# Performance work log

Measured on AMD Instinct MI355X. Metric: run time of the kernel, lower is better.

The kernel has to match this reference:

```python
import jax, jax.numpy as jnp
import numpy as np

B, T, C = 2, 2048, 768
H, D = 12, 64
INNER_LR = 0.01


def setup_inputs() -> dict:
    key = jax.random.key(0)
    ks = jax.random.split(key, 5)
    s = 1.0 / np.sqrt(C)
    return {
        "x": jax.random.normal(ks[0], (B, T, C), dtype=jnp.float32),
        "Wq": jax.random.normal(ks[1], (C, C), dtype=jnp.float32) * s,
        "Wk": jax.random.normal(ks[2], (C, C), dtype=jnp.float32) * s,
        "Wv": jax.random.normal(ks[3], (C, C), dtype=jnp.float32) * s,
        "Wo": jax.random.normal(ks[4], (C, C), dtype=jnp.float32) * s,
        "lr_scale": jnp.ones((H, 1, 1), dtype=jnp.float32),
    }


def reference(x, Wq, Wk, Wv, Wo, lr_scale):
    b, t, c = x.shape
    # projections (nn.Linear: x @ W.T), split heads -> [T, B, H, D] for scan
    def proj(W):
        return (x @ W.T).reshape(b, t, H, D).transpose(1, 0, 2, 3)

    q, k, v = proj(Wq), proj(Wk), proj(Wv)
    eff_lr = (INNER_LR * lr_scale)[None]  # [1, H, 1, 1] broadcasts over [B,H,D,D]

    def step(W, qkv_t):
        q_t, k_t, v_t = qkv_t  # each [B, H, D]
        out_t = jnp.einsum('bhij,bhj->bhi', W, q_t)          # read BEFORE update
        err = jnp.einsum('bhij,bhj->bhi', W, k_t) - v_t      # inner-loss residual
        grad = err[..., :, None] * k_t[..., None, :]         # [B,H,D,D] outer product
        W_new = W - eff_lr * grad                            # one GD step on W
        return W_new, out_t

    W0 = jnp.zeros((b, H, D, D), dtype=x.dtype)
    _, outs = jax.lax.scan(step, W0, (q, k, v))              # outs: [T, B, H, D]
    out = outs.transpose(1, 0, 2, 3).reshape(b, t, c)
    return out @ Wo.T
```

## Files before the change

kernel.cpp:

```cpp
#include <hip/hip_runtime.h>

#define BB 2
#define TT 2048
#define CC 768
#define HH 12
#define DD 64
#define NN (BB*TT)
#define NQ (BB*HH*TT*DD)
#define WSZ (CC*CC)
#define NCH 32
#define CL 64
#define NCHUNKS (BB*HH*NCH)

typedef __attribute__((ext_vector_type(8))) short short8;
typedef __attribute__((ext_vector_type(8))) unsigned short ushort8;
typedef __attribute__((ext_vector_type(4))) float f32x4;
typedef unsigned short u16;

#define GLOAD16(g, l)                                                        \
    __builtin_amdgcn_global_load_lds(                                        \
        (const __attribute__((address_space(1))) void*)(g),                  \
        (__attribute__((address_space(3))) void*)(l), 16, 0, 0)

__device__ __forceinline__ u16 f2b(float f) {
    unsigned int u = __builtin_bit_cast(unsigned int, f);
    unsigned int r = (u + 0x7FFFu + ((u >> 16) & 1u)) >> 16;
    return (u16)r;
}
__device__ __forceinline__ float b2f(u16 b) {
    unsigned int u = ((unsigned int)b) << 16;
    return __builtin_bit_cast(float, u);
}
template <int CTRL>
__device__ __forceinline__ float dpp_xadd(float x) {
    int y = __builtin_amdgcn_update_dpp(0, __builtin_bit_cast(int, x),
                                        CTRL, 0xF, 0xF, true);
    return x + __builtin_bit_cast(float, y);
}
__device__ __forceinline__ void st_sw(u16* buf, int row, int col, u16 v) {
    buf[row * 64 + ((((col >> 3) ^ (row & 7)) << 3) | (col & 7))] = v;
}
__device__ __forceinline__ short8 ld_frag(const u16* buf, int row, int lc) {
    return *(const short8*)&buf[row * 64 + ((lc ^ (row & 7)) << 3)];
}
__device__ __forceinline__ short8 gfrag(const u16* base, int row, int lc) {
    return *(const short8*)&base[row * 64 + lc * 8];
}

__global__ __launch_bounds__(256) void cvt5_kernel(
    const float* __restrict__ x,  const float* __restrict__ Wq,
    const float* __restrict__ Wk, const float* __restrict__ Wv,
    const float* __restrict__ Wo,
    u16* __restrict__ xb, u16* __restrict__ wqb, u16* __restrict__ wkb,
    u16* __restrict__ wvb, u16* __restrict__ wob)
{
    const int seg = blockIdx.y;
    const float* s; u16* d; int n8;
    if      (seg == 0) { s = x;  d = xb;  n8 = NQ  / 8; }
    else if (seg == 1) { s = Wq; d = wqb; n8 = WSZ / 8; }
    else if (seg == 2) { s = Wk; d = wkb; n8 = WSZ / 8; }
    else if (seg == 3) { s = Wv; d = wvb; n8 = WSZ / 8; }
    else               { s = Wo; d = wob; n8 = WSZ / 8; }
    int i = blockIdx.x * 256 + threadIdx.x;
    if (i >= n8) return;
    const float* p = s + (size_t)i * 8;
    ushort8 o;
#pragma unroll
    for (int j = 0; j < 8; ++j) o[j] = f2b(p[j]);
    *(ushort8*)(d + (size_t)i * 8) = o;
}

__global__ __launch_bounds__(256) void proj_qkv_kernel(
    const u16* __restrict__ xb,
    const u16* __restrict__ wq, const u16* __restrict__ wk,
    const u16* __restrict__ wv,
    u16* __restrict__ qo, u16* __restrict__ ko, u16* __restrict__ vo)
{
    const int z = blockIdx.z;
    const u16* Bsel = (z == 0) ? wq : ((z == 1) ? wk : wv);
    u16* Osel       = (z == 0) ? qo : ((z == 1) ? ko : vo);

    const int m0 = blockIdx.x * 128;
    const int n0 = blockIdx.y * 128;
    const int tid = threadIdx.x, lane = tid & 63, wid = tid >> 6;
    const int wm = (wid >> 1) * 64, wn = (wid & 1) * 64;

    __shared__ u16 As[128 * 64];
    __shared__ u16 Bs[128 * 64];

    f32x4 acc[4][4];
#pragma unroll
    for (int a = 0; a < 4; ++a)
#pragma unroll
        for (int b = 0; b < 4; ++b) acc[a][b] = (f32x4){0.f, 0.f, 0.f, 0.f};

    for (int kt = 0; kt < CC; kt += 64) {
#pragma unroll
        for (int i = 0; i < 4; ++i) {
            int slot = i * 256 + tid;
            int row = slot >> 3, c = slot & 7;
            int gc = c ^ (row & 7);
            GLOAD16(xb   + (size_t)(m0 + row) * CC + kt + gc * 8,
                    (char*)As + slot * 16);
            GLOAD16(Bsel + (size_t)(n0 + row) * CC + kt + gc * 8,
                    (char*)Bs + slot * 16);
        }
        asm volatile("s_waitcnt vmcnt(0)" ::: "memory");
        __syncthreads();

#pragma unroll
        for (int kh = 0; kh < 2; ++kh) {
            short8 af[4], bf[4];
            const int lc = kh * 4 + (lane >> 4);
#pragma unroll
            for (int mi = 0; mi < 4; ++mi) {
                int row = wm + mi * 16 + (lane & 15);
                af[mi] = *(const short8*)((const char*)As + row * 128
                                          + ((lc ^ (row & 7)) * 16));
            }
#pragma unroll
            for (int ni = 0; ni < 4; ++ni) {
                int row = wn + ni * 16 + (lane & 15);
                bf[ni] = *(const short8*)((const char*)Bs + row * 128
                                          + ((lc ^ (row & 7)) * 16));
            }
#pragma unroll
            for (int mi = 0; mi < 4; ++mi)
#pragma unroll
                for (int ni = 0; ni < 4; ++ni)
                    acc[mi][ni] = __builtin_amdgcn_mfma_f32_16x16x32_bf16(
                        af[mi], bf[ni], acc[mi][ni], 0, 0, 0);
        }
        __syncthreads();
    }

#pragma unroll
    for (int mi = 0; mi < 4; ++mi) {
#pragma unroll
        for (int ni = 0; ni < 4; ++ni) {
            int n = n0 + wn + ni * 16 + (lane & 15);
            int mbase = m0 + wm + mi * 16 + ((lane >> 4) << 2);
            int h = n >> 6, d = n & 63;
#pragma unroll
            for (int r = 0; r < 4; ++r) {
                int m = mbase + r;
                int b = m >> 11, t = m & 2047;
                Osel[(((size_t)b * HH + h) * TT + t) * DD + d] =
                    f2b(acc[mi][ni][r]);
            }
        }
    }
}

__global__ __launch_bounds__(256, 3) void ttt_prep3_kernel(
    const u16* __restrict__ kb, const u16* __restrict__ vb,
    const float* __restrict__ lr_scale,
    u16* __restrict__ ubg, float* __restrict__ pfA, float* __restrict__ pfB,
    u16* __restrict__ mtng, u16* __restrict__ rtng)
{
    const int bx = blockIdx.x;
    const int bh = bx >> 5;
    const int h = bh % HH;
    const float lr = 0.01f * lr_scale[h];
    const u16* kc = kb + (size_t)bx * 4096;
    const u16* vc = vb + (size_t)bx * 4096;
    u16* ubc  = ubg + (size_t)bx * 4096;
    float* pfc = (bx < 384) ? pfA + (size_t)bx * 4096
                            : pfB + (size_t)(bx - 384) * 4096;
    u16* mtnc = mtng + (size_t)bx * 4096;
    u16* rtnc = rtng + (size_t)bx * 4096;

    const int tid = threadIdx.x, lane = tid & 63, wid = tid >> 6;
    const int wm = (wid >> 1) * 32, wn = (wid & 1) * 32;
    const int ar0 = wm + (lane & 15);
    const int br0 = wn + (lane & 15);
    const int lcb = lane >> 4;
    const int or0 = wm + ((lane >> 4) << 2);
    const int oc0 = wn + (lane & 15);

    __shared__ __align__(16) char pool[50176];
    u16* Kl  = (u16*)pool;
    u16* Vl  = (u16*)(pool + 8192);
    u16* KtB = (u16*)(pool + 16384);
    u16* VtB = (u16*)(pool + 24576);
    float (*As)[68] = (float (*)[68])(pool + 32768);
    u16* Rb   = Kl;
    u16* Ub   = Vl;
    u16* TmpB = VtB;
    u16* Tb   = (u16*)(pool + 32768);
    u16* TmpA = (u16*)(pool + 40960);

#pragma unroll
    for (int i = 0; i < 2; ++i) {
        int slot = i * 256 + tid;
        int row = slot >> 3, cc = slot & 7;
        int gc = cc ^ (row & 7);
        GLOAD16(kc + row * 64 + gc * 8, (char*)Kl + slot * 16);
        GLOAD16(vc + row * 64 + gc * 8, (char*)Vl + slot * 16);
    }
    asm volatile("s_waitcnt vmcnt(0)" ::: "memory");
    __syncthreads();

    {
        short8 idA[2][2];
#pragma unroll
        for (int mi = 0; mi < 2; ++mi)
#pragma unroll
            for (int kh = 0; kh < 2; ++kh) {
                short8 idf = {0, 0, 0, 0, 0, 0, 0, 0};
#pragma unroll
                for (int e = 0; e < 8; ++e)
                    if (kh * 32 + lcb * 8 + e == ar0 + mi * 16)
                        idf[e] = (short)0x3F80;
                idA[mi][kh] = idf;
            }

        f32x4 aA[2][2], aKt[2][2], aVt[2][2];
#pragma unroll
        for (int a = 0; a < 2; ++a)
#pragma unroll
            for (int b = 0; b < 2; ++b) {
                aA[a][b]  = (f32x4){0.f, 0.f, 0.f, 0.f};
                aKt[a][b] = (f32x4){0.f, 0.f, 0.f, 0.f};
                aVt[a][b] = (f32x4){0.f, 0.f, 0.f, 0.f};
            }
#pragma unroll
        for (int kh = 0; kh < 2; ++kh) {
            short8 ka[2], kbb[2], vbb[2];
#pragma unroll
            for (int i = 0; i < 2; ++i) {
                ka[i]  = ld_frag(Kl, ar0 + i * 16, kh * 4 + lcb);
                kbb[i] = ld_frag(Kl, br0 + i * 16, kh * 4 + lcb);
                vbb[i] = ld_frag(Vl, br0 + i * 16, kh * 4 + lcb);
            }
#pragma unroll
            for (int mi = 0; mi < 2; ++mi)
#pragma unroll
                for (int ni = 0; ni < 2; ++ni) {
                    aA[mi][ni] = __builtin_amdgcn_mfma_f32_16x16x32_bf16(
                        ka[mi], kbb[ni], aA[mi][ni], 0, 0, 0);
                    aKt[mi][ni] = __builtin_amdgcn_mfma_f32_16x16x32_bf16(
                        idA[mi][kh], kbb[ni], aKt[mi][ni], 0, 0, 0);
                    aVt[mi][ni] = __builtin_amdgcn_mfma_f32_16x16x32_bf16(
                        idA[mi][kh], vbb[ni], aVt[mi][ni], 0, 0, 0);
                }
        }
#pragma unroll
        for (int mi = 0; mi < 2; ++mi)
#pragma unroll
            for (int ni = 0; ni < 2; ++ni)
#pragma unroll
                for (int r = 0; r < 4; ++r) {
                    int t = or0 + mi * 16 + r, s = oc0 + ni * 16;
                    As[t][s] = (t > s) ? lr * aA[mi][ni][r] : 0.f;
                    st_sw(KtB, t, s, f2b(aKt[mi][ni][r]));
                    st_sw(VtB, t, s, f2b(aVt[mi][ni][r]));
                }
    }
    __syncthreads();

    const int j = wid * 16 + (lane >> 2), g = lane & 3;
    float Treg[16];
#pragma unroll
    for (int m = 0; m < 16; ++m) Treg[m] = 0.f;
#pragma unroll
    for (int t = 0; t < 64; ++t) {
        float sum = 0.f;
#pragma unroll
        for (int m = 0; m <= (t >> 2); ++m)
            sum += As[t][g + 4 * m] * Treg[m];
        sum = dpp_xadd<0xB1>(sum);
        sum = dpp_xadd<0x4E>(sum);
        float v = ((t == j) ? 1.f : 0.f) - sum;
        if ((t & 3) == g) Treg[t >> 2] = v;
    }
    __syncthreads();

#pragma unroll
    for (int m = 0; m < 16; ++m) st_sw(Tb, g + 4 * m, j, f2b(Treg[m]));
    __syncthreads();

    {
        f32x4 aR[2][2], aU[2][2], aRt[2][2];
#pragma unroll
        for (int a = 0; a < 2; ++a)
#pragma unroll
            for (int b = 0; b < 2; ++b) {
                aR[a][b]  = (f32x4){0.f, 0.f, 0.f, 0.f};
                aU[a][b]  = (f32x4){0.f, 0.f, 0.f, 0.f};
                aRt[a][b] = (f32x4){0.f, 0.f, 0.f, 0.f};
            }
#pragma unroll
        for (int kh = 0; kh < 2; ++kh) {
            short8 kta[2], vta[2], ta[2], tbf[2], ktb[2];
#pragma unroll
            for (int i = 0; i < 2; ++i) {
                kta[i] = ld_frag(KtB, ar0 + i * 16, kh * 4 + lcb);
                vta[i] = ld_frag(VtB, ar0 + i * 16, kh * 4 + lcb);
                ta[i]  = ld_frag(Tb,  ar0 + i * 16, kh * 4 + lcb);
                tbf[i] = ld_frag(Tb,  br0 + i * 16, kh * 4 + lcb);
                ktb[i] = ld_frag(KtB, br0 + i * 16, kh * 4 + lcb);
            }
#pragma unroll
            for (int mi = 0; mi < 2; ++mi)
#pragma unroll
                for (int ni = 0; ni < 2; ++ni) {
                    aR[mi][ni] = __builtin_amdgcn_mfma_f32_16x16x32_bf16(
                        kta[mi], tbf[ni], aR[mi][ni], 0, 0, 0);
                    aU[mi][ni] = __builtin_amdgcn_mfma_f32_16x16x32_bf16(
                        vta[mi], tbf[ni], aU[mi][ni], 0, 0, 0);
                    aRt[mi][ni] = __builtin_amdgcn_mfma_f32_16x16x32_bf16(
                        ta[mi], ktb[ni], aRt[mi][ni], 0, 0, 0);
                }
        }
#pragma unroll
        for (int mi = 0; mi < 2; ++mi)
#pragma unroll
            for (int ni = 0; ni < 2; ++ni) {
                u16 ue[4];
#pragma unroll
                for (int r = 0; r < 4; ++r) {
                    int ro = or0 + mi * 16 + r, co = oc0 + ni * 16;
                    st_sw(Rb, ro, co, f2b(lr * aR[mi][ni][r]));
                    ue[r] = f2b(lr * aU[mi][ni][r]);
                    st_sw(Ub, ro, co, ue[r]);
                    st_sw(TmpA, ro, co, f2b(-lr * aRt[mi][ni][r]));
                }
                uint2 uo;
                uo.x = (unsigned)ue[0] | ((unsigned)ue[1] << 16);
                uo.y = (unsigned)ue[2] | ((unsigned)ue[3] << 16);
                *(uint2*)&ubc[(size_t)((((wid * 2 + mi) * 2 + ni) * 64
                                        + lane) * 4)] = uo;
            }
    }
    __syncthreads();

    {
        f32x4 aM[2][2], aP[2][2];
#pragma unroll
        for (int a = 0; a < 2; ++a)
#pragma unroll
            for (int b = 0; b < 2; ++b) {
                aM[a][b] = (f32x4){0.f, 0.f, 0.f, 0.f};
                aP[a][b] = (f32x4){0.f, 0.f, 0.f, 0.f};
            }
#pragma unroll
        for (int kh = 0; kh < 2; ++kh) {
            short8 kta[2], ua[2], rbb[2], ktb[2];
#pragma unroll
            for (int i = 0; i < 2; ++i) {
                kta[i] = ld_frag(KtB, ar0 + i * 16, kh * 4 + lcb);
                ua[i]  = ld_frag(Ub,  ar0 + i * 16, kh * 4 + lcb);
                rbb[i] = ld_frag(Rb,  br0 + i * 16, kh * 4 + lcb);
                ktb[i] = ld_frag(KtB, br0 + i * 16, kh * 4 + lcb);
            }
#pragma unroll
            for (int mi = 0; mi < 2; ++mi)
#pragma unroll
                for (int ni = 0; ni < 2; ++ni) {
                    aM[mi][ni] = __builtin_amdgcn_mfma_f32_16x16x32_bf16(
                        kta[mi], rbb[ni], aM[mi][ni], 0, 0, 0);
                    aP[mi][ni] = __builtin_amdgcn_mfma_f32_16x16x32_bf16(
                        ua[mi], ktb[ni], aP[mi][ni], 0, 0, 0);
                }
        }
#pragma unroll
        for (int mi = 0; mi < 2; ++mi)
#pragma unroll
            for (int ni = 0; ni < 2; ++ni) {
#pragma unroll
                for (int r = 0; r < 4; ++r)
                    st_sw(TmpB, or0 + mi * 16 + r, oc0 + ni * 16,
                          f2b(-aM[mi][ni][r]));
                *(f32x4*)&pfc[(size_t)((((wid * 2 + mi) * 2 + ni) * 64
                                        + lane) * 4)] = aP[mi][ni];
            }
    }
    if (wid < 2) {
#pragma unroll
        for (int ni = 0; ni < 2; ++ni)
#pragma unroll
            for (int kh = 0; kh < 2; ++kh) {
                short8 v = ld_frag(TmpA, (wid & 1) * 32 + ni * 16 + (lane & 15),
                                   kh * 4 + lcb);
                *(short8*)&rtnc[(size_t)(((((wid & 1) * 2 + ni) * 2 + kh) * 64
                                          + lane) * 8)] = v;
            }
    }
    __syncthreads();
    if (wid < 2) {
#pragma unroll
        for (int ni = 0; ni < 2; ++ni)
#pragma unroll
            for (int kh = 0; kh < 2; ++kh) {
                short8 v = ld_frag(TmpB, (wid & 1) * 32 + ni * 16 + (lane & 15),
                                   kh * 4 + lcb);
                *(short8*)&mtnc[(size_t)(((((wid & 1) * 2 + ni) * 2 + kh) * 64
                                          + lane) * 8)] = v;
            }
    }
}

__global__ __launch_bounds__(256, 1) void ttt_seq_kernel(
    u16* __restrict__ mtnW, const float* __restrict__ pfA,
    const float* __restrict__ pfB)
{
    const int bh = blockIdx.x;
    const int bx0 = bh * NCH;
    const int tid = threadIdx.x, lane = tid & 63, wid = tid >> 6;
    const int wm = (wid >> 1) * 32, wn = (wid & 1) * 32;
    const int ar0 = wm + (lane & 15);
    const int lcb = lane >> 4;
    const int or0 = wm + ((lane >> 4) << 2);
    const int oc0 = wn + (lane & 15);
    const int wn2 = wid & 1;

    __shared__ u16 Wb[4096];

    f32x4 accW[2][2];
#pragma unroll
    for (int a = 0; a < 2; ++a)
#pragma unroll
        for (int b = 0; b < 2; ++b) accW[a][b] = (f32x4){0.f, 0.f, 0.f, 0.f};

    auto ldMtn = [&](int c, short8 (&m)[2][2]) {
        const u16* mb = mtnW + (size_t)(bx0 + c) * 4096;
#pragma unroll
        for (int ni = 0; ni < 2; ++ni)
#pragma unroll
            for (int kh = 0; kh < 2; ++kh)
                m[ni][kh] = *(const short8*)&mb[(size_t)(
                    (((wn2 * 2 + ni) * 2 + kh) * 64 + lane) * 8)];
    };
    auto ldPf = [&](int c, f32x4 (&p)[2][2]) {
        int bx = bx0 + c;
        const float* pb = (bx < 384) ? pfA + (size_t)bx * 4096
                                     : pfB + (size_t)(bx - 384) * 4096;
#pragma unroll
        for (int mi = 0; mi < 2; ++mi)
#pragma unroll
            for (int ni = 0; ni < 2; ++ni)
                p[mi][ni] = *(const f32x4*)&pb[(size_t)(
                    (((wid * 2 + mi) * 2 + ni) * 64 + lane) * 4)];
    };

    auto body = [&](int c, short8 (&cm)[2][2], f32x4 (&cp)[2][2],
                    short8 (&nm)[2][2], f32x4 (&np)[2][2]) {
        asm volatile("s_waitcnt vmcnt(0)" ::: "memory");
        u16* wcp = mtnW + (size_t)(bx0 + c) * 4096;
#pragma unroll
        for (int mi = 0; mi < 2; ++mi)
#pragma unroll
            for (int ni = 0; ni < 2; ++ni)
#pragma unroll
                for (int r = 0; r < 4; ++r) {
                    u16 v = f2b(accW[mi][ni][r]);
                    wcp[(or0 + mi * 16 + r) * 64 + oc0 + ni * 16] = v;
                    st_sw(Wb, or0 + mi * 16 + r, oc0 + ni * 16, v);
                }
        if (c + 1 < NCH) { ldMtn(c + 1, nm); ldPf(c + 1, np); }
        __syncthreads();
        short8 wf[2][2];
#pragma unroll
        for (int mi = 0; mi < 2; ++mi)
#pragma unroll
            for (int kh = 0; kh < 2; ++kh)
                wf[mi][kh] = ld_frag(Wb, ar0 + mi * 16, kh * 4 + lcb);
#pragma unroll
        for (int mi = 0; mi < 2; ++mi)
#pragma unroll
            for (int ni = 0; ni < 2; ++ni) {
                f32x4 d = cp[mi][ni];
#pragma unroll
                for (int kh = 0; kh < 2; ++kh)
                    d = __builtin_amdgcn_mfma_f32_16x16x32_bf16(
                        wf[mi][kh], cm[ni][kh], d, 0, 0, 0);
                accW[mi][ni] = accW[mi][ni] + d;
            }
        __syncthreads();
    };

    short8 mA[2][2], mB[2][2];
    f32x4 pA[2][2], pB[2][2];
    ldMtn(0, mA); ldPf(0, pA);
    for (int c = 0; c < NCH; c += 2) {
        body(c,     mA, pA, mB, pB);
        body(c + 1, mB, pB, mA, pA);
    }
}

__global__ __launch_bounds__(256) void ttt_outgen_kernel(
    const u16* __restrict__ qb, const u16* __restrict__ kb,
    const u16* __restrict__ wcg, const u16* __restrict__ rtng,
    const u16* __restrict__ ubg, u16* __restrict__ hid)
{
    const int bx = blockIdx.x;
    const int bh = bx >> 5, c = bx & 31;
    const int b = bh / HH, h = bh % HH;
    const u16* qc = qb + (size_t)bx * 4096;
    const u16* kc = kb + (size_t)bx * 4096;
    const u16* wcc = wcg + (size_t)bx * 4096;
    const u16* rtnc = rtng + (size_t)bx * 4096;
    const u16* ubc = ubg + (size_t)bx * 4096;
    u16* hch = hid + (size_t)b * TT * CC + h * DD;

    const int tid = threadIdx.x, lane = tid & 63, wid = tid >> 6;
    const int wm = (wid >> 1) * 32, wn = (wid & 1) * 32;
    const int ar0 = wm + (lane & 15);
    const int br0 = wn + (lane & 15);
    const int lcb = lane >> 4;
    const int or0 = wm + ((lane >> 4) << 2);
    const int oc0 = wn + (lane & 15);
    const int wn2 = wid & 1;

    __shared__ u16 Sl[4096], El[4096];

    short8 Qa[2][2], Kb2[2][2];
#pragma unroll
    for (int i = 0; i < 2; ++i)
#pragma unroll
        for (int kh = 0; kh < 2; ++kh) {
            Qa[i][kh]  = gfrag(qc, ar0 + i * 16, kh * 4 + lcb);
            Kb2[i][kh] = gfrag(kc, br0 + i * 16, kh * 4 + lcb);
        }
    f32x4 aS[2][2];
#pragma unroll
    for (int a = 0; a < 2; ++a)
#pragma unroll
        for (int d = 0; d < 2; ++d) aS[a][d] = (f32x4){0.f, 0.f, 0.f, 0.f};
#pragma unroll
    for (int kh = 0; kh < 2; ++kh)
#pragma unroll
        for (int mi = 0; mi < 2; ++mi)
#pragma unroll
            for (int ni = 0; ni < 2; ++ni)
                aS[mi][ni] = __builtin_amdgcn_mfma_f32_16x16x32_bf16(
                    Qa[mi][kh], Kb2[ni][kh], aS[mi][ni], 0, 0, 0);
#pragma unroll
    for (int mi = 0; mi < 2; ++mi)
#pragma unroll
        for (int ni = 0; ni < 2; ++ni)
#pragma unroll
            for (int r = 0; r < 4; ++r) {
                int t = or0 + mi * 16 + r, s = oc0 + ni * 16;
                st_sw(Sl, t, s, f2b((t > s) ? aS[mi][ni][r] : 0.f));
            }

    f32x4 aE[2][2];
#pragma unroll
    for (int mi = 0; mi < 2; ++mi)
#pragma unroll
        for (int ni = 0; ni < 2; ++ni) {
            uint2 uu = *(const uint2*)&ubc[(size_t)(
                (((wid * 2 + mi) * 2 + ni) * 64 + lane) * 4)];
            f32x4 e;
            e[0] = b2f((u16)(uu.x & 0xFFFF)); e[1] = b2f((u16)(uu.x >> 16));
            e[2] = b2f((u16)(uu.y & 0xFFFF)); e[3] = b2f((u16)(uu.y >> 16));
            aE[mi][ni] = e;
        }
    short8 Wa[2][2], Rtb[2][2];
#pragma unroll
    for (int i = 0; i < 2; ++i)
#pragma unroll
        for (int kh = 0; kh < 2; ++kh) {
            Wa[i][kh] = gfrag(wcc, ar0 + i * 16, kh * 4 + lcb);
            Rtb[i][kh] = *(const short8*)&rtnc[(size_t)(
                (((wn2 * 2 + i) * 2 + kh) * 64 + lane) * 8)];
        }
#pragma unroll
    for (int kh = 0; kh < 2; ++kh)
#pragma unroll
        for (int mi = 0; mi < 2; ++mi)
#pragma unroll
            for (int ni = 0; ni < 2; ++ni)
                aE[mi][ni] = __builtin_amdgcn_mfma_f32_16x16x32_bf16(
                    Wa[mi][kh], Rtb[ni][kh], aE[mi][ni], 0, 0, 0);
#pragma unroll
    for (int mi = 0; mi < 2; ++mi)
#pragma unroll
        for (int ni = 0; ni < 2; ++ni)
#pragma unroll
            for (int r = 0; r < 4; ++r)
                st_sw(El, or0 + mi * 16 + r, oc0 + ni * 16,
                      f2b(aE[mi][ni][r]));
    __syncthreads();

    f32x4 aO[2][2];
#pragma unroll
    for (int a = 0; a < 2; ++a)
#pragma unroll
        for (int d = 0; d < 2; ++d) aO[a][d] = (f32x4){0.f, 0.f, 0.f, 0.f};
#pragma unroll
    for (int kh = 0; kh < 2; ++kh) {
        short8 Wb2[2], Sa[2], Eb[2];
#pragma unroll
        for (int i = 0; i < 2; ++i) {
            Wb2[i] = gfrag(wcc, br0 + i * 16, kh * 4 + lcb);
            Sa[i]  = ld_frag(Sl, ar0 + i * 16, kh * 4 + lcb);
            Eb[i]  = ld_frag(El, br0 + i * 16, kh * 4 + lcb);
        }
#pragma unroll
        for (int mi = 0; mi < 2; ++mi)
#pragma unroll
            for (int ni = 0; ni < 2; ++ni) {
                aO[mi][ni] = __builtin_amdgcn_mfma_f32_16x16x32_bf16(
                    Qa[mi][kh], Wb2[ni], aO[mi][ni], 0, 0, 0);
                aO[mi][ni] = __builtin_amdgcn_mfma_f32_16x16x32_bf16(
                    Sa[mi], Eb[ni], aO[mi][ni], 0, 0, 0);
            }
    }
#pragma unroll
    for (int mi = 0; mi < 2; ++mi)
#pragma unroll
        for (int ni = 0; ni < 2; ++ni)
#pragma unroll
            for (int r = 0; r < 4; ++r)
                hch[(size_t)(c * CL + or0 + mi * 16 + r) * CC
                    + oc0 + ni * 16] = f2b(aO[mi][ni][r]);
}

__global__ __launch_bounds__(256) void out_proj_kernel(
    const u16* __restrict__ hid, const u16* __restrict__ wo,
    float* __restrict__ out)
{
    const int m0 = blockIdx.x * 128;
    const int n0 = blockIdx.y * 128;
    const int tid = threadIdx.x, lane = tid & 63, wid = tid >> 6;
    const int wm = (wid >> 1) * 64, wn = (wid & 1) * 64;

    __shared__ u16 As[128 * 64];
    __shared__ u16 Bs[128 * 64];

    f32x4 acc[4][4];
#pragma unroll
    for (int a = 0; a < 4; ++a)
#pragma unroll
        for (int b = 0; b < 4; ++b) acc[a][b] = (f32x4){0.f, 0.f, 0.f, 0.f};

    for (int kt = 0; kt < CC; kt += 64) {
#pragma unroll
        for (int i = 0; i < 4; ++i) {
            int slot = i * 256 + tid;
            int row = slot >> 3, c = slot & 7;
            int gc = c ^ (row & 7);
            GLOAD16(hid + (size_t)(m0 + row) * CC + kt + gc * 8,
                    (char*)As + slot * 16);
            GLOAD16(wo  + (size_t)(n0 + row) * CC + kt + gc * 8,
                    (char*)Bs + slot * 16);
        }
        asm volatile("s_waitcnt vmcnt(0)" ::: "memory");
        __syncthreads();

#pragma unroll
        for (int kh = 0; kh < 2; ++kh) {
            short8 af[4], bf[4];
            const int lc = kh * 4 + (lane >> 4);
#pragma unroll
            for (int mi = 0; mi < 4; ++mi) {
                int row = wm + mi * 16 + (lane & 15);
                af[mi] = *(const short8*)((const char*)As + row * 128
                                          + ((lc ^ (row & 7)) * 16));
            }
#pragma unroll
            for (int ni = 0; ni < 4; ++ni) {
                int row = wn + ni * 16 + (lane & 15);
                bf[ni] = *(const short8*)((const char*)Bs + row * 128
                                          + ((lc ^ (row & 7)) * 16));
            }
#pragma unroll
            for (int mi = 0; mi < 4; ++mi)
#pragma unroll
                for (int ni = 0; ni < 4; ++ni)
                    acc[mi][ni] = __builtin_amdgcn_mfma_f32_16x16x32_bf16(
                        af[mi], bf[ni], acc[mi][ni], 0, 0, 0);
        }
        __syncthreads();
    }

#pragma unroll
    for (int mi = 0; mi < 4; ++mi) {
#pragma unroll
        for (int ni = 0; ni < 4; ++ni) {
            int n = n0 + wn + ni * 16 + (lane & 15);
            int mbase = m0 + wm + mi * 16 + ((lane >> 4) << 2);
#pragma unroll
            for (int r = 0; r < 4; ++r)
                out[(size_t)(mbase + r) * CC + n] = acc[mi][ni][r];
        }
    }
}

extern "C" void kernel_launch(void* const* d_in, const int* in_sizes, int n_in,
                              void* d_out, int out_size, void* d_ws, size_t ws_size,
                              hipStream_t stream) {
    const float* x  = (const float*)d_in[0];
    const float* Wq = (const float*)d_in[1];
    const float* Wk = (const float*)d_in[2];
    const float* Wv = (const float*)d_in[3];
    const float* Wo = (const float*)d_in[4];
    const float* lr = (const float*)d_in[5];

    u16* us   = (u16*)d_ws;
    u16* qb   = us;
    u16* kbw  = us + (size_t)NQ;
    u16* vbw  = us + (size_t)2 * NQ;
    u16* xb   = us + (size_t)3 * NQ;
    u16* mtnW = us + (size_t)4 * NQ;
    u16* rtn  = us + (size_t)5 * NQ;
    float* pfB = (float*)(us + (size_t)6 * NQ);
    u16* wqb = us + (size_t)7 * NQ;
    u16* wkb = wqb + WSZ;
    u16* wvb = wkb + WSZ;
    u16* wob = wvb + WSZ;
    u16* ub  = vbw;
    float* pfA = (float*)xb;
    u16* hid = xb;

    cvt5_kernel<<<dim3((NQ / 8 + 255) / 256, 5), 256, 0, stream>>>(
        x, Wq, Wk, Wv, Wo, xb, wqb, wkb, wvb, wob);

    proj_qkv_kernel<<<dim3(NN / 128, CC / 128, 3), 256, 0, stream>>>(
        xb, wqb, wkb, wvb, qb, kbw, vbw);

    ttt_prep3_kernel<<<dim3(NCHUNKS), 256, 0, stream>>>(
        kbw, vbw, lr, ub, pfA, pfB, mtnW, rtn);

    ttt_seq_kernel<<<dim3(BB * HH), 256, 0, stream>>>(mtnW, pfA, pfB);

    ttt_outgen_kernel<<<dim3(NCHUNKS), 256, 0, stream>>>(
        qb, kbw, mtnW, rtn, ub, hid);

    out_proj_kernel<<<dim3(NN / 128, CC / 128), 256, 0, stream>>>(
        hid, wob, (float*)d_out);
}
```

Measured before the change: 103.5 us.

## Double-buffer GEMM LDS tiles and sequential W buffer to overlap loads

Both projection GEMMs now use two LDS buffers per operand, prefetching the next k-tile with global_load_lds while computing the current one (waitcnt vmcnt(8) lets the newer loads stay in flight). The sequential TTT kernel ping-pongs its W staging buffer, which removes one barrier per chunk step. The chunk-prep epilogue is restructured so TmpA and TmpB are written out by different waves in parallel after a single barrier. LDS per block doubles in the GEMMs, which can lower occupancy.

```diff
diff --git a/kernel.cpp b/kernel.cpp
--- a/kernel.cpp
+++ b/kernel.cpp
@@ -85,8 +85,8 @@
     const int tid = threadIdx.x, lane = tid & 63, wid = tid >> 6;
     const int wm = (wid >> 1) * 64, wn = (wid & 1) * 64;
 
-    __shared__ u16 As[128 * 64];
-    __shared__ u16 Bs[128 * 64];
+    __shared__ u16 As[2][128 * 64];
+    __shared__ u16 Bs[2][128 * 64];
 
     f32x4 acc[4][4];
 #pragma unroll
@@ -94,18 +94,29 @@
 #pragma unroll
         for (int b = 0; b < 4; ++b) acc[a][b] = (f32x4){0.f, 0.f, 0.f, 0.f};
 
-    for (int kt = 0; kt < CC; kt += 64) {
+    auto stage = [&](int buf, int kt) {
 #pragma unroll
         for (int i = 0; i < 4; ++i) {
             int slot = i * 256 + tid;
             int row = slot >> 3, c = slot & 7;
             int gc = c ^ (row & 7);
             GLOAD16(xb   + (size_t)(m0 + row) * CC + kt + gc * 8,
-                    (char*)As + slot * 16);
+                    (char*)&As[buf][0] + slot * 16);
             GLOAD16(Bsel + (size_t)(n0 + row) * CC + kt + gc * 8,
-                    (char*)Bs + slot * 16);
-        }
-        asm volatile("s_waitcnt vmcnt(0)" ::: "memory");
+                    (char*)&Bs[buf][0] + slot * 16);
+        }
+    };
+
+    stage(0, 0);
+    int cur = 0;
+    const int NK = CC / 64;
+    for (int it = 0; it < NK; ++it) {
+        if (it + 1 < NK) {
+            stage(cur ^ 1, (it + 1) * 64);
+            asm volatile("s_waitcnt vmcnt(8)" ::: "memory");
+        } else {
+            asm volatile("s_waitcnt vmcnt(0)" ::: "memory");
+        }
         __syncthreads();
 
 #pragma unroll
@@ -115,13 +126,13 @@
 #pragma unroll
             for (int mi = 0; mi < 4; ++mi) {
                 int row = wm + mi * 16 + (lane & 15);
-                af[mi] = *(const short8*)((const char*)As + row * 128
+                af[mi] = *(const short8*)((const char*)&As[cur][0] + row * 128
                                           + ((lc ^ (row & 7)) * 16));
             }
 #pragma unroll
             for (int ni = 0; ni < 4; ++ni) {
                 int row = wn + ni * 16 + (lane & 15);
-                bf[ni] = *(const short8*)((const char*)Bs + row * 128
+                bf[ni] = *(const short8*)((const char*)&Bs[cur][0] + row * 128
                                           + ((lc ^ (row & 7)) * 16));
             }
 #pragma unroll
@@ -132,6 +143,7 @@
                         af[mi], bf[ni], acc[mi][ni], 0, 0, 0);
         }
         __syncthreads();
+        cur ^= 1;
     }
 
 #pragma unroll
@@ -376,7 +388,18 @@
                                         + lane) * 4)] = aP[mi][ni];
             }
     }
+    __syncthreads();
     if (wid < 2) {
+#pragma unroll
+        for (int ni = 0; ni < 2; ++ni)
+#pragma unroll
+            for (int kh = 0; kh < 2; ++kh) {
+                short8 v = ld_frag(TmpB, (wid & 1) * 32 + ni * 16 + (lane & 15),
+                                   kh * 4 + lcb);
+                *(short8*)&mtnc[(size_t)(((((wid & 1) * 2 + ni) * 2 + kh) * 64
+                                          + lane) * 8)] = v;
+            }
+    } else {
 #pragma unroll
         for (int ni = 0; ni < 2; ++ni)
 #pragma unroll
@@ -384,18 +407,6 @@
                 short8 v = ld_frag(TmpA, (wid & 1) * 32 + ni * 16 + (lane & 15),
                                    kh * 4 + lcb);
                 *(short8*)&rtnc[(size_t)(((((wid & 1) * 2 + ni) * 2 + kh) * 64
-                                          + lane) * 8)] = v;
-            }
-    }
-    __syncthreads();
-    if (wid < 2) {
-#pragma unroll
-        for (int ni = 0; ni < 2; ++ni)
-#pragma unroll
-            for (int kh = 0; kh < 2; ++kh) {
-                short8 v = ld_frag(TmpB, (wid & 1) * 32 + ni * 16 + (lane & 15),
-                                   kh * 4 + lcb);
-                *(short8*)&mtnc[(size_t)(((((wid & 1) * 2 + ni) * 2 + kh) * 64
                                           + lane) * 8)] = v;
             }
     }
@@ -415,7 +426,7 @@
     const int oc0 = wn + (lane & 15);
     const int wn2 = wid & 1;
 
-    __shared__ u16 Wb[4096];
+    __shared__ u16 Wb[2][4096];
 
     f32x4 accW[2][2];
 #pragma unroll
@@ -448,6 +459,7 @@
                     short8 (&nm)[2][2], f32x4 (&np)[2][2]) {
         asm volatile("s_waitcnt vmcnt(0)" ::: "memory");
         u16* wcp = mtnW + (size_t)(bx0 + c) * 4096;
+        u16* wl = &Wb[c & 1][0];
 #pragma unroll
         for (int mi = 0; mi < 2; ++mi)
 #pragma unroll
@@ -456,7 +468,7 @@
                 for (int r = 0; r < 4; ++r) {
                     u16 v = f2b(accW[mi][ni][r]);
                     wcp[(or0 + mi * 16 + r) * 64 + oc0 + ni * 16] = v;
-                    st_sw(Wb, or0 + mi * 16 + r, oc0 + ni * 16, v);
+                    st_sw(wl, or0 + mi * 16 + r, oc0 + ni * 16, v);
                 }
         if (c + 1 < NCH) { ldMtn(c + 1, nm); ldPf(c + 1, np); }
         __syncthreads();
@@ -465,7 +477,7 @@
         for (int mi = 0; mi < 2; ++mi)
 #pragma unroll
             for (int kh = 0; kh < 2; ++kh)
-                wf[mi][kh] = ld_frag(Wb, ar0 + mi * 16, kh * 4 + lcb);
+                wf[mi][kh] = ld_frag(wl, ar0 + mi * 16, kh * 4 + lcb);
 #pragma unroll
         for (int mi = 0; mi < 2; ++mi)
 #pragma unroll
@@ -477,7 +489,6 @@
                         wf[mi][kh], cm[ni][kh], d, 0, 0, 0);
                 accW[mi][ni] = accW[mi][ni] + d;
             }
-        __syncthreads();
     };
 
     short8 mA[2][2], mB[2][2];
@@ -628,8 +639,8 @@
     const int tid = threadIdx.x, lane = tid & 63, wid = tid >> 6;
     const int wm = (wid >> 1) * 64, wn = (wid & 1) * 64;
 
-    __shared__ u16 As[128 * 64];
-    __shared__ u16 Bs[128 * 64];
+    __shared__ u16 As[2][128 * 64];
+    __shared__ u16 Bs[2][128 * 64];
 
     f32x4 acc[4][4];
 #pragma unroll
@@ -637,18 +648,29 @@
 #pragma unroll
         for (int b = 0; b < 4; ++b) acc[a][b] = (f32x4){0.f, 0.f, 0.f, 0.f};
 
-    for (int kt = 0; kt < CC; kt += 64) {
+    auto stage = [&](int buf, int kt) {
 #pragma unroll
         for (int i = 0; i < 4; ++i) {
             int slot = i * 256 + tid;
             int row = slot >> 3, c = slot & 7;
             int gc = c ^ (row & 7);
             GLOAD16(hid + (size_t)(m0 + row) * CC + kt + gc * 8,
-                    (char*)As + slot * 16);
+                    (char*)&As[buf][0] + slot * 16);
             GLOAD16(wo  + (size_t)(n0 + row) * CC + kt + gc * 8,
-                    (char*)Bs + slot * 16);
-        }
-        asm volatile("s_waitcnt vmcnt(0)" ::: "memory");
+                    (char*)&Bs[buf][0] + slot * 16);
+        }
+    };
+
+    stage(0, 0);
+    int cur = 0;
+    const int NK = CC / 64;
+    for (int it = 0; it < NK; ++it) {
+        if (it + 1 < NK) {
+            stage(cur ^ 1, (it + 1) * 64);
+            asm volatile("s_waitcnt vmcnt(8)" ::: "memory");
+        } else {
+            asm volatile("s_waitcnt vmcnt(0)" ::: "memory");
+        }
         __syncthreads();
 
 #pragma unroll
@@ -658,13 +680,13 @@
 #pragma unroll
             for (int mi = 0; mi < 4; ++mi) {
                 int row = wm + mi * 16 + (lane & 15);
-                af[mi] = *(const short8*)((const char*)As + row * 128
+                af[mi] = *(const short8*)((const char*)&As[cur][0] + row * 128
                                           + ((lc ^ (row & 7)) * 16));
             }
 #pragma unroll
             for (int ni = 0; ni < 4; ++ni) {
                 int row = wn + ni * 16 + (lane & 15);
-                bf[ni] = *(const short8*)((const char*)Bs + row * 128
+                bf[ni] = *(const short8*)((const char*)&Bs[cur][0] + row * 128
                                           + ((lc ^ (row & 7)) * 16));
             }
 #pragma unroll
@@ -675,6 +697,7 @@
                         af[mi], bf[ni], acc[mi][ni], 0, 0, 0);
         }
         __syncthreads();
+        cur ^= 1;
     }
 
 #pragma unroll
```

Result: no change. 105.3 us (+1.7%).
